# Optimization experiments

Hardware: AMD Instinct MI355X
Metric: run time of the kernel (lower is better)

## Reference

```python
import jax, jax.numpy as jnp
import numpy as np

# graph metadata: 3 node types, 4 canonical etypes
NT_SRC = (0, 1, 1, 2)   # src ntype of each relation
NT_DST = (1, 0, 2, 1)   # dst ntype of each relation
GROUPS = {0: (1,), 1: (0, 3), 2: (2,)}  # relations sharing each dst ntype (in dict order)
NEG_SLOPE = 0.2
N_NODES, N_EDGES, IN_DIM = 50000, 200000, 256
HEADS, HID = 8, 32
REL_IN, REL_HID = 64, 32


def _leaky(x):
    return jax.nn.leaky_relu(x, NEG_SLOPE)


def _segment_softmax(e, seg, n):
    # numerically stable softmax over edges grouped by dst node
    m = jax.ops.segment_max(e, seg, num_segments=n)
    ex = jnp.exp(e - m[seg])
    s = jax.ops.segment_sum(ex, seg, num_segments=n)
    return ex / s[seg]


def setup_inputs() -> dict:
    key = jax.random.key(0)
    ks = jax.random.split(key, 12)
    w = 0.05  # xavier-like scale
    feat = jax.random.normal(ks[0], (4, N_NODES, IN_DIM), jnp.float32)
    rel_emb = jax.random.normal(ks[1], (4, REL_IN), jnp.float32)
    node_W = jax.random.normal(ks[2], (3, IN_DIM, HEADS * HID), jnp.float32) * w
    rel_W = jax.random.normal(ks[3], (4, REL_IN, HEADS * 2 * HID), jnp.float32) * w
    res_W = jax.random.normal(ks[4], (3, IN_DIM, HEADS * HID), jnp.float32) * w
    res_b = jnp.zeros((3, HEADS * HID), jnp.float32)
    res_alpha = jax.random.normal(ks[5], (3,), jnp.float32)
    cross_attn = jax.random.normal(ks[6], (4, HEADS, HID), jnp.float32) * w
    prop_W = jax.random.normal(ks[7], (4, REL_IN, HEADS * REL_HID), jnp.float32) * w
    prop_b = jnp.zeros((4, HEADS * REL_HID), jnp.float32)
    src_idx = jax.random.randint(ks[8], (4, N_EDGES), 0, N_NODES, jnp.int32)
    dst_idx = jax.random.randint(ks[9], (4, N_EDGES), 0, N_NODES, jnp.int32)
    return dict(feat=feat, rel_emb=rel_emb, node_W=node_W, rel_W=rel_W,
                res_W=res_W, res_b=res_b, res_alpha=res_alpha,
                cross_attn=cross_attn, prop_W=prop_W, prop_b=prop_b,
                src_idx=src_idx, dst_idx=dst_idx)


def reference(feat, rel_emb, node_W, rel_W, res_W, res_b, res_alpha,
              cross_attn, prop_W, prop_b, src_idx, dst_idx):
    R, N, _ = feat.shape
    H, D = HEADS, HID
    conv_out = []
    for r in range(R):  # fixed small set of relations
        s, d = NT_SRC[r], NT_DST[r]
        # RelationGraphConv (dropout is identity in eval)
        fsrc = (feat[r] @ node_W[s]).reshape(N, H, D)
        fdst = (feat[r] @ node_W[d]).reshape(N, H, D)
        ra = (rel_emb[r] @ rel_W[r]).reshape(H, 2 * D)
        e_dst = (fdst * ra[:, :D]).sum(-1)           # (N, H)
        e_src = (fsrc * ra[:, D:]).sum(-1)           # (N, H)
        e = _leaky(e_src[src_idx[r]] + e_dst[dst_idx[r]])  # (E, H)
        a = _segment_softmax(e, dst_idx[r], N)       # edge softmax per dst node
        msg = fsrc[src_idx[r]] * a[:, :, None]       # (E, H, D)
        out = jax.ops.segment_sum(msg, dst_idx[r], num_segments=N)
        out = jax.nn.relu(out.reshape(N, H * D))
        # residual gate
        alpha = jax.nn.sigmoid(res_alpha[d])
        out = out * alpha + (feat[r] @ res_W[d] + res_b[d]) * (1.0 - alpha)
        conv_out.append(out)
    # RelationCrossing over relations sharing the dst ntype
    node_out = []
    for r in range(R):
        group = GROUPS[NT_DST[r]]
        if len(group) == 1:
            node_out.append(conv_out[group[0]])
        else:
            stacked = jnp.stack([conv_out[g] for g in group], 0).reshape(len(group), N, H, D)
            att = _leaky((stacked * cross_attn[r]).sum(-1, keepdims=True))  # (Rg, N, H, 1)
            att = jax.nn.softmax(att, axis=0)
            node_out.append((stacked * att).sum(0).reshape(N, H * D))
    node_out = jnp.stack(node_out, 0)                # (4, N, H*D)
    # relation embedding propagation
    rel_out = jnp.einsum('ri,rio->ro', rel_emb, prop_W) + prop_b  # (4, H*rel_hid)
    return node_out, rel_out
```

## Files before the change

### kernel.cpp

```cpp
#include <hip/hip_runtime.h>
#include <hip/hip_bf16.h>
#include <stdint.h>

typedef unsigned int u32;
typedef unsigned short u16;
typedef short short8 __attribute__((ext_vector_type(8)));
typedef float f32x4 __attribute__((ext_vector_type(4)));
typedef unsigned short u16x4 __attribute__((ext_vector_type(4)));
typedef __attribute__((address_space(1))) const u32 gu32;
typedef __attribute__((address_space(3))) u32 lu32;

#define NN 50000
#define NE 200000
#define WCT 576

__device__ __forceinline__ float leaky(float x){ return x >= 0.f ? x : 0.2f*x; }
__device__ __forceinline__ float bf2f(u16 u){ return __uint_as_float(((u32)u)<<16); }
__device__ __forceinline__ u16 f2bf(float f){
    u32 u = __float_as_uint(f);
    u32 r = (u + 0x7fffu + ((u>>16)&1u)) >> 16;
    return (u16)r;
}
__device__ __forceinline__ u32 pack_bf2(float a, float b){
    return __builtin_amdgcn_perm(__float_as_uint(b), __float_as_uint(a), 0x07060302u);
}
__device__ __forceinline__ int nt_src(int r){ return (r==0)?0:((r==3)?2:1); }
__device__ __forceinline__ int nt_dst(int r){ return (r==1)?0:((r==2)?2:1); }

__global__ void k_ra(const float* __restrict__ rel_emb, const float* __restrict__ rel_W,
                     float* __restrict__ ra){
    int r = blockIdx.x;
    for (int j = threadIdx.x; j < 512; j += blockDim.x){
        float acc = 0.f;
        for (int i = 0; i < 64; i++) acc += rel_emb[r*64+i] * rel_W[(r*64+i)*512 + j];
        ra[r*512 + j] = acc;
    }
}

__global__ void k_wcat(const float* __restrict__ node_W, const float* __restrict__ res_W,
                       const float* __restrict__ ra, u16* __restrict__ WcatS){
    int g = blockIdx.x*blockDim.x + threadIdx.x;
    if (g >= 4*WCT*256) return;
    int r = g/147456; int rem = g%147456;
    int tile = rem/16384; int rem2 = rem%16384;
    int kc = rem2/512; int rem3 = rem2%512;
    int nrow = rem3>>3; int off = rem3&7;
    int n = tile*64 + nrow;
    int k = kc*8 + off;
    int s = nt_src(r), d = nt_dst(r);
    float v;
    if (n < 256) v = node_W[(s*256+k)*256 + n];
    else if (n < 512) v = res_W[(d*256+k)*256 + (n-256)];
    else if (n < 520){
        int h = n-512; float a = 0.f;
        for (int dd = 0; dd < 32; dd++) a += node_W[(s*256+k)*256 + h*32+dd] * ra[r*512 + h*64+32+dd];
        v = a;
    } else if (n < 528){
        int h = n-520; float a = 0.f;
        for (int dd = 0; dd < 32; dd++) a += node_W[(d*256+k)*256 + h*32+dd] * ra[r*512 + h*64+dd];
        v = a;
    } else v = 0.f;
    WcatS[g] = f2bf(v);
}

__launch_bounds__(512, 4)
__global__ void k_gemm(const float* __restrict__ feat, const u16* __restrict__ WcatS,
                       const float* __restrict__ res_b,
                       u16* __restrict__ fsrc, u16* __restrict__ resb,
                       float* __restrict__ e_comb){
    __shared__ uint4 lsB[4096];
    const short8* lsB8 = (const short8*)lsB;

    int r = blockIdx.y;
    int row0 = blockIdx.x*128;
    const float* A = feat + (size_t)r*NN*256;
    const u16*   W = WcatS + (size_t)r*9*16384;

    int t = threadIdx.x;
    int w = t>>6, l = t&63;
    int wm = (w>>1)*32, wn = (w&1)*32;
    int li = l & 15, lg = l >> 4;

    short8 afr[2][8];
    #pragma unroll
    for (int mt = 0; mt < 2; mt++){
        int grow = row0 + wm + mt*16 + li; if (grow > NN-1) grow = NN-1;
        const float* ap = A + (size_t)grow*256 + lg*8;
        #pragma unroll
        for (int kk = 0; kk < 8; kk++){
            f32x4 x = __builtin_nontemporal_load((const f32x4*)(ap + kk*32));
            f32x4 y = __builtin_nontemporal_load((const f32x4*)(ap + kk*32 + 4));
            short8 f;
            ((u32*)&f)[0] = pack_bf2(x.x, x.y);
            ((u32*)&f)[1] = pack_bf2(x.z, x.w);
            ((u32*)&f)[2] = pack_bf2(y.x, y.y);
            ((u32*)&f)[3] = pack_bf2(y.z, y.w);
            afr[mt][kk] = f;
        }
    }

    #pragma unroll
    for (int i = 0; i < 4; i++){
        int chunk = i*512 + t;
        __builtin_amdgcn_global_load_lds((gu32*)(W + (size_t)chunk*8),
                                         (lu32*)((char*)lsB + chunk*16), 16, 0, 0);
    }
    __syncthreads();

    int d = nt_dst(r);
    int orow = t>>2, oq = t&3;
    int ogrow = row0 + orow;
    size_t onidx = (size_t)r*NN + ogrow;

    for (int T = 0; T < 8; T++){
        int cur = T & 1;
        {
            const u16* tb = W + (size_t)(T+1)*16384;
            char* lb = (char*)lsB + (cur^1)*32768;
            #pragma unroll
            for (int i = 0; i < 4; i++){
                int chunk = i*512 + t;
                __builtin_amdgcn_global_load_lds((gu32*)(tb + (size_t)chunk*8),
                                                 (lu32*)(lb + chunk*16), 16, 0, 0);
            }
        }
        f32x4 acc[2][2] = {};
        #pragma unroll
        for (int kk = 0; kk < 8; kk++){
            short8 bfr[2];
            #pragma unroll
            for (int nt = 0; nt < 2; nt++)
                bfr[nt] = lsB8[cur*2048 + (kk*4+lg)*64 + wn + nt*16 + li];
            #pragma unroll
            for (int mt = 0; mt < 2; mt++)
                #pragma unroll
                for (int nt = 0; nt < 2; nt++)
                    acc[mt][nt] = __builtin_amdgcn_mfma_f32_16x16x32_bf16(afr[mt][kk], bfr[nt], acc[mt][nt], 0,0,0);
        }
        float bias[2] = {0.f, 0.f};
        if (T >= 4){
            bias[0] = res_b[d*256 + (T-4)*64 + wn + li];
            bias[1] = res_b[d*256 + (T-4)*64 + wn + 16 + li];
        }
        __syncthreads();
        u16* cst = (u16*)(lsB + (size_t)cur*2048);
        #pragma unroll
        for (int mt = 0; mt < 2; mt++)
            #pragma unroll
            for (int nt = 0; nt < 2; nt++)
                #pragma unroll
                for (int qq = 0; qq < 4; qq++)
                    cst[(wm + mt*16 + lg*4 + qq)*72 + wn + nt*16 + li] = f2bf(acc[mt][nt][qq] + bias[nt]);
        __syncthreads();
        if (ogrow < NN){
            u16* dst = (T < 4) ? (fsrc + onidx*256 + T*64) : (resb + onidx*256 + (T-4)*64);
            const uint4* src = (const uint4*)(cst + orow*72 + oq*16);
            uint4* dq = (uint4*)(dst + oq*16);
            dq[0] = src[0];
            dq[1] = src[1];
        }
        __syncthreads();
    }

    if (wn == 0){
        f32x4 acc[2] = {};
        #pragma unroll
        for (int kk = 0; kk < 8; kk++){
            short8 bfr = lsB8[(kk*4+lg)*64 + li];
            #pragma unroll
            for (int mt = 0; mt < 2; mt++)
                acc[mt] = __builtin_amdgcn_mfma_f32_16x16x32_bf16(afr[mt][kk], bfr, acc[mt], 0,0,0);
        }
        #pragma unroll
        for (int mt = 0; mt < 2; mt++)
            #pragma unroll
            for (int qq = 0; qq < 4; qq++){
                int row = row0 + wm + mt*16 + lg*4 + qq;
                if (row < NN)
                    e_comb[((size_t)r*NN + row)*16 + li] = acc[mt][qq];
            }
    }
}


__global__ void k_count(const int* __restrict__ dst_idx, u32* __restrict__ cnt){
    int r = blockIdx.y; int e = blockIdx.x*256 + threadIdx.x;
    if (e >= NE) return;
    atomicAdd(&cnt[r*NN + dst_idx[r*NE+e]], 1u);
}

__global__ void k_scan1(const u32* __restrict__ cnt, u32* __restrict__ bsum){
    int r = blockIdx.y, b = blockIdx.x;
    int i = b*256 + threadIdx.x;
    u32 v = (i < NN) ? cnt[r*NN+i] : 0u;
    #pragma unroll
    for (int off = 1; off < 64; off <<= 1) v += __shfl_xor(v, off, 64);
    __shared__ u32 wsum[4];
    int lane = threadIdx.x & 63, w = threadIdx.x >> 6;
    if (lane == 0) wsum[w] = v;
    __syncthreads();
    if (threadIdx.x == 0) bsum[r*256 + b] = wsum[0]+wsum[1]+wsum[2]+wsum[3];
}

__device__ __forceinline__ u32 block_scan_incl(u32 v){
    __shared__ u32 wsum[4];
    int lane = threadIdx.x & 63, w = threadIdx.x >> 6;
    #pragma unroll
    for (int off = 1; off < 64; off <<= 1){
        u32 t = __shfl_up(v, off, 64);
        if (lane >= off) v += t;
    }
    if (lane == 63) wsum[w] = v;
    __syncthreads();
    u32 add = 0;
    #pragma unroll
    for (int k = 0; k < 4; k++) if (k < w) add += wsum[k];
    return v + add;
}

__global__ void k_scan2(u32* __restrict__ bsum){
    int r = blockIdx.x;
    u32 v = bsum[r*256 + threadIdx.x];
    u32 incl = block_scan_incl(v);
    bsum[r*256 + threadIdx.x] = incl - v;
}

__global__ void k_scan3(const u32* __restrict__ cnt, const u32* __restrict__ bsum,
                        u32* __restrict__ row_ptr){
    int r = blockIdx.y, b = blockIdx.x;
    int i = b*256 + threadIdx.x;
    u32 v = (i < NN) ? cnt[r*NN+i] : 0u;
    u32 incl = block_scan_incl(v);
    if (i < NN) row_ptr[r*(NN+1) + i + 1] = bsum[r*256 + b] + incl;
    if (b == 0 && threadIdx.x == 0) row_ptr[r*(NN+1)] = 0u;
}

__global__ void k_scatter(const int* __restrict__ src_idx, const int* __restrict__ dst_idx,
                          const float* __restrict__ e_comb,
                          const u32* __restrict__ row_ptr, u32* __restrict__ cnt2,
                          u32* __restrict__ src_pack, float* __restrict__ e_pack){
    int r = blockIdx.y; int e = blockIdx.x*256 + threadIdx.x;
    if (e >= NE) return;
    int s = src_idx[r*NE+e], d = dst_idx[r*NE+e];
    u32 pos = row_ptr[r*(NN+1)+d] + atomicAdd(&cnt2[r*NN+d], 1u);
    src_pack[r*NE + pos] = (u32)s;
    const f32x4* es = (const f32x4*)(e_comb + (size_t)(r*NN+s)*16);
    const f32x4* ed = (const f32x4*)(e_comb + (size_t)(r*NN+d)*16 + 8);
    f32x4 s0 = es[0], s1 = es[1], d0 = ed[0], d1 = ed[1];
    f32x4 w0, w1;
    w0.x = __expf(leaky(s0.x+d0.x)); w0.y = __expf(leaky(s0.y+d0.y));
    w0.z = __expf(leaky(s0.z+d0.z)); w0.w = __expf(leaky(s0.w+d0.w));
    w1.x = __expf(leaky(s1.x+d1.x)); w1.y = __expf(leaky(s1.y+d1.y));
    w1.z = __expf(leaky(s1.z+d1.z)); w1.w = __expf(leaky(s1.w+d1.w));
    f32x4* ep = (f32x4*)(e_pack + ((size_t)(r*NE)+pos)*8);
    ep[0] = w0; ep[1] = w1;
}

__device__ __forceinline__ void agg_core(int n, int r, int l, int h,
                                         const u32* __restrict__ row_ptr,
                                         const u32* __restrict__ src_pack,
                                         const float* __restrict__ e_pack,
                                         const u16* __restrict__ fsrc,
                                         const u16* __restrict__ resb,
                                         const float* __restrict__ res_alpha,
                                         float& c0, float& c1, float& c2, float& c3){
    u32 p0 = row_ptr[r*(NN+1)+n];
    u32 p1 = row_ptr[r*(NN+1)+n+1];
    int deg = (int)(p1 - p0);

    float s = 0.f;
    float a0=0.f, a1=0.f, a2=0.f, a3=0.f;
    const size_t ebase = (size_t)r*NE + p0;
    const u16* fbase = fsrc + (size_t)r*NN*256;
    for (int base = 0; base < deg; base += 64){
        int rem = deg - base; if (rem > 64) rem = 64;
        u32 my_src = 0;
        if (l < rem) my_src = src_pack[ebase + base + l];
        int i = 0;
        for (; i+4 <= rem; i += 4){
            u32 s0 = __shfl(my_src, i, 64);
            u32 s1 = __shfl(my_src, i+1, 64);
            u32 s2 = __shfl(my_src, i+2, 64);
            u32 s3 = __shfl(my_src, i+3, 64);
            float ex0 = e_pack[(ebase + base + i)*8 + h];
            float ex1 = e_pack[(ebase + base + i + 1)*8 + h];
            float ex2 = e_pack[(ebase + base + i + 2)*8 + h];
            float ex3 = e_pack[(ebase + base + i + 3)*8 + h];
            ushort4 f0 = *(const ushort4*)(fbase + (size_t)s0*256 + l*4);
            ushort4 f1 = *(const ushort4*)(fbase + (size_t)s1*256 + l*4);
            ushort4 f2 = *(const ushort4*)(fbase + (size_t)s2*256 + l*4);
            ushort4 f3 = *(const ushort4*)(fbase + (size_t)s3*256 + l*4);
            s += ex0 + ex1 + ex2 + ex3;
            a0 += bf2f(f0.x)*ex0 + bf2f(f1.x)*ex1 + bf2f(f2.x)*ex2 + bf2f(f3.x)*ex3;
            a1 += bf2f(f0.y)*ex0 + bf2f(f1.y)*ex1 + bf2f(f2.y)*ex2 + bf2f(f3.y)*ex3;
            a2 += bf2f(f0.z)*ex0 + bf2f(f1.z)*ex1 + bf2f(f2.z)*ex2 + bf2f(f3.z)*ex3;
            a3 += bf2f(f0.w)*ex0 + bf2f(f1.w)*ex1 + bf2f(f2.w)*ex2 + bf2f(f3.w)*ex3;
        }
        for (; i < rem; i++){
            u32 s0 = __shfl(my_src, i, 64);
            float ex0 = e_pack[(ebase + base + i)*8 + h];
            ushort4 f0 = *(const ushort4*)(fbase + (size_t)s0*256 + l*4);
            s += ex0;
            a0 += bf2f(f0.x)*ex0; a1 += bf2f(f0.y)*ex0; a2 += bf2f(f0.z)*ex0; a3 += bf2f(f0.w)*ex0;
        }
    }
    float inv_sh = (deg > 0) ? 1.0f / s : 0.f;

    int d = nt_dst(r);
    float alpha = 1.f/(1.f + __expf(-res_alpha[d]));
    float beta = 1.f - alpha;
    u16x4 rv = __builtin_nontemporal_load((const u16x4*)(resb + ((size_t)r*NN+n)*256 + l*4));
    c0 = fmaxf(a0*inv_sh,0.f)*alpha + bf2f(rv.x)*beta;
    c1 = fmaxf(a1*inv_sh,0.f)*alpha + bf2f(rv.y)*beta;
    c2 = fmaxf(a2*inv_sh,0.f)*alpha + bf2f(rv.z)*beta;
    c3 = fmaxf(a3*inv_sh,0.f)*alpha + bf2f(rv.w)*beta;
}

__launch_bounds__(128)
__global__ void k_agg12(const u32* __restrict__ row_ptr, const u32* __restrict__ src_pack,
                        const float* __restrict__ e_pack, const u16* __restrict__ fsrc,
                        const u16* __restrict__ resb, const float* __restrict__ res_alpha,
                        float* __restrict__ out){
    int n = blockIdx.x;
    int r = 1 + (threadIdx.x >> 6);
    int l = threadIdx.x & 63;
    int h = l >> 3;
    float c0, c1, c2, c3;
    agg_core(n, r, l, h, row_ptr, src_pack, e_pack, fsrc, resb, res_alpha, c0, c1, c2, c3);
    f32x4 o = {c0, c1, c2, c3};
    __builtin_nontemporal_store(o, (f32x4*)(out + ((size_t)r*NN+n)*256 + l*4));
}

__launch_bounds__(128)
__global__ void k_aggx03(const u32* __restrict__ row_ptr, const u32* __restrict__ src_pack,
                         const float* __restrict__ e_pack, const u16* __restrict__ fsrc,
                         const u16* __restrict__ resb, const float* __restrict__ res_alpha,
                         const float* __restrict__ cross_attn, float* __restrict__ out){
    __shared__ float cbuf[2][256];
    __shared__ float dots[4][8];

    int n = blockIdx.x;
    int w = threadIdx.x >> 6;
    int r = w ? 3 : 0;
    int l = threadIdx.x & 63;
    int h = l >> 3;
    float c0, c1, c2, c3;
    agg_core(n, r, l, h, row_ptr, src_pack, e_pack, fsrc, resb, res_alpha, c0, c1, c2, c3);

    int slot = w;
    cbuf[slot][l*4+0] = c0; cbuf[slot][l*4+1] = c1;
    cbuf[slot][l*4+2] = c2; cbuf[slot][l*4+3] = c3;
    const float* ca0 = cross_attn;
    const float* ca3 = cross_attn + 3*256;
    float d0 = c0*ca0[l*4+0] + c1*ca0[l*4+1] + c2*ca0[l*4+2] + c3*ca0[l*4+3];
    float d3 = c0*ca3[l*4+0] + c1*ca3[l*4+1] + c2*ca3[l*4+2] + c3*ca3[l*4+3];
    #pragma unroll
    for (int msk = 1; msk < 8; msk <<= 1){
        d0 += __shfl_xor(d0, msk, 64);
        d3 += __shfl_xor(d3, msk, 64);
    }
    if ((l & 7) == 0){
        dots[slot*2+0][h] = d0;
        dots[slot*2+1][h] = d3;
    }
    __syncthreads();
    float g0 = (r == 0) ? dots[0][h] : dots[1][h];
    float g3 = (r == 0) ? dots[2][h] : dots[3][h];
    g0 = leaky(g0); g3 = leaky(g3);
    float mm = fmaxf(g0, g3);
    float w0 = __expf(g0-mm), w3 = __expf(g3-mm);
    float inv = 1.f/(w0+w3);
    w0 *= inv; w3 *= inv;
    f32x4 o;
    o.x = w0*cbuf[0][l*4+0] + w3*cbuf[1][l*4+0];
    o.y = w0*cbuf[0][l*4+1] + w3*cbuf[1][l*4+1];
    o.z = w0*cbuf[0][l*4+2] + w3*cbuf[1][l*4+2];
    o.w = w0*cbuf[0][l*4+3] + w3*cbuf[1][l*4+3];
    __builtin_nontemporal_store(o, (f32x4*)(out + ((size_t)r*NN+n)*256 + l*4));
}

__global__ void k_relout(const float* __restrict__ rel_emb, const float* __restrict__ prop_W,
                         const float* __restrict__ prop_b, float* __restrict__ out){
    int r = blockIdx.x; int o = threadIdx.x;
    float acc = prop_b[r*256 + o];
    for (int i = 0; i < 64; i++) acc += rel_emb[r*64+i] * prop_W[(r*64+i)*256 + o];
    out[(size_t)4*NN*256 + r*256 + o] = acc;
}

extern "C" void kernel_launch(void* const* d_in, const int* in_sizes, int n_in,
                              void* d_out, int out_size, void* d_ws, size_t ws_size,
                              hipStream_t stream){
    const float* feat      = (const float*)d_in[0];
    const float* rel_emb   = (const float*)d_in[1];
    const float* node_W    = (const float*)d_in[2];
    const float* rel_W     = (const float*)d_in[3];
    const float* res_W     = (const float*)d_in[4];
    const float* res_b     = (const float*)d_in[5];
    const float* res_alpha = (const float*)d_in[6];
    const float* cross_attn= (const float*)d_in[7];
    const float* prop_W    = (const float*)d_in[8];
    const float* prop_b    = (const float*)d_in[9];
    const int* src_idx     = (const int*)d_in[10];
    const int* dst_idx     = (const int*)d_in[11];
    float* out = (float*)d_out;

    char* ws = (char*)d_ws;
    u32*   cnt     = (u32*)  (ws);
    u32*   cnt2    = (u32*)  (ws + 800000);
    u32*   bsum    = (u32*)  (ws + 1600000);
    u32*   row_ptr = (u32*)  (ws + 1604096);
    float* ra      = (float*)(ws + 2404112);
    u16*   WcatS   = (u16*)  (ws + 2412304);
    float* e_comb  = (float*)(ws + 3591952);
    u32*   src_pack= (u32*)  (ws + 16391952);
    float* e_pack  = (float*)(ws + 19591952);
    u16*   fsrc    = (u16*)  (ws + 45191952);
    u16*   resb    = (u16*)  (ws + 147591952);

    hipMemsetAsync(cnt, 0, 1604096, stream);

    k_ra<<<4, 256, 0, stream>>>(rel_emb, rel_W, ra);
    k_wcat<<<(4*WCT*256)/256, 256, 0, stream>>>(node_W, res_W, ra, WcatS);
    dim3 gg((NN+127)/128, 4);
    k_gemm<<<gg, 512, 0, stream>>>(feat, WcatS, res_b, fsrc, resb, e_comb);

    dim3 geg((NE+255)/256, 4);
    k_count<<<geg, 256, 0, stream>>>(dst_idx, cnt);
    dim3 gsc((NN+255)/256, 4);
    k_scan1<<<gsc, 256, 0, stream>>>(cnt, bsum);
    k_scan2<<<4, 256, 0, stream>>>(bsum);
    k_scan3<<<gsc, 256, 0, stream>>>(cnt, bsum, row_ptr);
    k_scatter<<<geg, 256, 0, stream>>>(src_idx, dst_idx, e_comb, row_ptr, cnt2,
                                       src_pack, e_pack);
    k_agg12<<<NN, 128, 0, stream>>>(row_ptr, src_pack, e_pack, fsrc, resb,
                                    res_alpha, out);
    k_aggx03<<<NN, 128, 0, stream>>>(row_ptr, src_pack, e_pack, fsrc, resb,
                                     res_alpha, cross_attn, out);
    k_relout<<<4, 256, 0, stream>>>(rel_emb, prop_W, prop_b, out);
}
```

Measured before the change: 415.6 us.

## Shrink GEMM N-tile to 32 columns and warp tile to 16x32 for occupancy

The weight matrix is relaid out into 18 slabs of 32 columns instead of 9 of 64, which halves the LDS B buffer and lets each wave own a 16-row by 32-column tile. The attention-score columns become a 17th pass of the same loop instead of a separate tail. Launch bounds go from 4 to 6 blocks so more waves can hide memory latency. In exchange each B fragment is reused across fewer rows, and there are twice as many loop iterations, each with three barriers and narrower 16-byte output stores.

```diff
diff --git a/kernel.cpp b/kernel.cpp
--- a/kernel.cpp
+++ b/kernel.cpp
@@ -42,10 +42,10 @@
     int g = blockIdx.x*blockDim.x + threadIdx.x;
     if (g >= 4*WCT*256) return;
     int r = g/147456; int rem = g%147456;
-    int tile = rem/16384; int rem2 = rem%16384;
-    int kc = rem2/512; int rem3 = rem2%512;
+    int s9 = rem/8192; int rem2 = rem%8192;
+    int kc = rem2/256; int rem3 = rem2%256;
     int nrow = rem3>>3; int off = rem3&7;
-    int n = tile*64 + nrow;
+    int n = s9*32 + nrow;
     int k = kc*8 + off;
     int s = nt_src(r), d = nt_dst(r);
     float v;
@@ -63,28 +63,27 @@
     WcatS[g] = f2bf(v);
 }
 
-__launch_bounds__(512, 4)
+__launch_bounds__(512, 6)
 __global__ void k_gemm(const float* __restrict__ feat, const u16* __restrict__ WcatS,
                        const float* __restrict__ res_b,
                        u16* __restrict__ fsrc, u16* __restrict__ resb,
                        float* __restrict__ e_comb){
-    __shared__ uint4 lsB[4096];
+    __shared__ uint4 lsB[2048];
     const short8* lsB8 = (const short8*)lsB;
 
     int r = blockIdx.y;
     int row0 = blockIdx.x*128;
     const float* A = feat + (size_t)r*NN*256;
-    const u16*   W = WcatS + (size_t)r*9*16384;
+    const u16*   W = WcatS + (size_t)r*18*8192;
 
     int t = threadIdx.x;
     int w = t>>6, l = t&63;
-    int wm = (w>>1)*32, wn = (w&1)*32;
+    int wm = w*16;
     int li = l & 15, lg = l >> 4;
 
-    short8 afr[2][8];
-    #pragma unroll
-    for (int mt = 0; mt < 2; mt++){
-        int grow = row0 + wm + mt*16 + li; if (grow > NN-1) grow = NN-1;
+    short8 afr[8];
+    {
+        int grow = row0 + wm + li; if (grow > NN-1) grow = NN-1;
         const float* ap = A + (size_t)grow*256 + lg*8;
         #pragma unroll
         for (int kk = 0; kk < 8; kk++){
@@ -95,12 +94,12 @@
             ((u32*)&f)[1] = pack_bf2(x.z, x.w);
             ((u32*)&f)[2] = pack_bf2(y.x, y.y);
             ((u32*)&f)[3] = pack_bf2(y.z, y.w);
-            afr[mt][kk] = f;
+            afr[kk] = f;
         }
     }
 
     #pragma unroll
-    for (int i = 0; i < 4; i++){
+    for (int i = 0; i < 2; i++){
         int chunk = i*512 + t;
         __builtin_amdgcn_global_load_lds((gu32*)(W + (size_t)chunk*8),
                                          (lu32*)((char*)lsB + chunk*16), 16, 0, 0);
@@ -112,73 +111,53 @@
     int ogrow = row0 + orow;
     size_t onidx = (size_t)r*NN + ogrow;
 
-    for (int T = 0; T < 8; T++){
-        int cur = T & 1;
-        {
-            const u16* tb = W + (size_t)(T+1)*16384;
-            char* lb = (char*)lsB + (cur^1)*32768;
+    for (int s = 0; s < 17; s++){
+        int cur = s & 1;
+        if (s < 16){
+            const u16* tb = W + (size_t)(s+1)*8192;
+            char* lb = (char*)lsB + (cur^1)*16384;
             #pragma unroll
-            for (int i = 0; i < 4; i++){
+            for (int i = 0; i < 2; i++){
                 int chunk = i*512 + t;
                 __builtin_amdgcn_global_load_lds((gu32*)(tb + (size_t)chunk*8),
                                                  (lu32*)(lb + chunk*16), 16, 0, 0);
             }
         }
-        f32x4 acc[2][2] = {};
+        f32x4 acc[2] = {};
         #pragma unroll
         for (int kk = 0; kk < 8; kk++){
-            short8 bfr[2];
-            #pragma unroll
-            for (int nt = 0; nt < 2; nt++)
-                bfr[nt] = lsB8[cur*2048 + (kk*4+lg)*64 + wn + nt*16 + li];
-            #pragma unroll
-            for (int mt = 0; mt < 2; mt++)
-                #pragma unroll
-                for (int nt = 0; nt < 2; nt++)
-                    acc[mt][nt] = __builtin_amdgcn_mfma_f32_16x16x32_bf16(afr[mt][kk], bfr[nt], acc[mt][nt], 0,0,0);
-        }
-        float bias[2] = {0.f, 0.f};
-        if (T >= 4){
-            bias[0] = res_b[d*256 + (T-4)*64 + wn + li];
-            bias[1] = res_b[d*256 + (T-4)*64 + wn + 16 + li];
-        }
-        __syncthreads();
-        u16* cst = (u16*)(lsB + (size_t)cur*2048);
-        #pragma unroll
-        for (int mt = 0; mt < 2; mt++)
+            short8 b0 = lsB8[cur*1024 + (kk*4+lg)*32 + li];
+            short8 b1 = lsB8[cur*1024 + (kk*4+lg)*32 + 16 + li];
+            acc[0] = __builtin_amdgcn_mfma_f32_16x16x32_bf16(afr[kk], b0, acc[0], 0,0,0);
+            acc[1] = __builtin_amdgcn_mfma_f32_16x16x32_bf16(afr[kk], b1, acc[1], 0,0,0);
+        }
+        if (s < 16){
+            float bias[2] = {0.f, 0.f};
+            if (s >= 8){
+                bias[0] = res_b[d*256 + (s-8)*32 + li];
+                bias[1] = res_b[d*256 + (s-8)*32 + 16 + li];
+            }
+            __syncthreads();
+            u16* cst = (u16*)(lsB + (size_t)cur*1024);
             #pragma unroll
             for (int nt = 0; nt < 2; nt++)
                 #pragma unroll
                 for (int qq = 0; qq < 4; qq++)
-                    cst[(wm + mt*16 + lg*4 + qq)*72 + wn + nt*16 + li] = f2bf(acc[mt][nt][qq] + bias[nt]);
-        __syncthreads();
-        if (ogrow < NN){
-            u16* dst = (T < 4) ? (fsrc + onidx*256 + T*64) : (resb + onidx*256 + (T-4)*64);
-            const uint4* src = (const uint4*)(cst + orow*72 + oq*16);
-            uint4* dq = (uint4*)(dst + oq*16);
-            dq[0] = src[0];
-            dq[1] = src[1];
-        }
-        __syncthreads();
-    }
-
-    if (wn == 0){
-        f32x4 acc[2] = {};
-        #pragma unroll
-        for (int kk = 0; kk < 8; kk++){
-            short8 bfr = lsB8[(kk*4+lg)*64 + li];
-            #pragma unroll
-            for (int mt = 0; mt < 2; mt++)
-                acc[mt] = __builtin_amdgcn_mfma_f32_16x16x32_bf16(afr[mt][kk], bfr, acc[mt], 0,0,0);
-        }
-        #pragma unroll
-        for (int mt = 0; mt < 2; mt++)
+                    cst[(wm + lg*4 + qq)*36 + nt*16 + li] = f2bf(acc[nt][qq] + bias[nt]);
+            __syncthreads();
+            if (ogrow < NN){
+                u16* dst = (s < 8) ? (fsrc + onidx*256 + s*32) : (resb + onidx*256 + (s-8)*32);
+                *(uint4*)(dst + oq*8) = *(const uint4*)(cst + orow*36 + oq*8);
+            }
+            __syncthreads();
+        } else {
             #pragma unroll
             for (int qq = 0; qq < 4; qq++){
-                int row = row0 + wm + mt*16 + lg*4 + qq;
+                int row = row0 + wm + lg*4 + qq;
                 if (row < NN)
-                    e_comb[((size_t)r*NN + row)*16 + li] = acc[mt][qq];
+                    e_comb[((size_t)r*NN + row)*16 + li] = acc[0][qq];
             }
+        }
     }
 }
 
```

Result: faster. 405.4 us, median of 2 (-2.4%).
